# Optimization experiments

Measured on AMD Instinct MI355X. Metric: run time of the kernel, lower is better.

The kernel has to match this reference:

```python
import jax, jax.numpy as jnp
import numpy as np

SR = 4  # search_range
D = 2 * SR + 1  # 9
NC = D * D      # 81 output channels


def setup_inputs() -> dict:
    key = jax.random.key(0)
    k1, k2 = jax.random.split(key)
    B, C, H, W = 8, 64, 192, 256
    x1 = jax.random.normal(k1, (B, C, H, W), dtype=jnp.float32)
    x2 = jax.random.normal(k2, (B, C, H, W), dtype=jnp.float32)
    return {"x1": x1, "x2": x2}


def reference(x1, x2):
    B, C, H, W = x1.shape
    # Zero-pad x2 so out-of-overlap products are zero, matching the
    # zero-initialized cv in the original module.
    x2p = jnp.pad(x2, ((0, 0), (0, 0), (SR, SR), (SR, SR)))
    outs = [None] * NC
    for i in range(-SR, SR + 1):
        for j in range(-SR, SR + 1):
            # Original torch code uses cv[:, 9*i + j] with negative wraparound.
            k = (D * i + j) % NC
            # x2 sample position is (h - i, w - j); in padded coords start = SR - i.
            shifted = jax.lax.dynamic_slice(
                x2p, (0, 0, SR - i, SR - j), (B, C, H, W))
            outs[k] = jnp.sum(x1 * shifted, axis=1)  # [B, H, W]
    cv = jnp.stack(outs, axis=1)  # [B, 81, H, W]
    return cv / NC
```

## Files before the change

### kernel.cpp

```cpp
#include <hip/hip_runtime.h>

#define HH 192
#define WW 256
#define TH 8
#define TW 32
#define CCH 4
#define NCHUNK 16
#define THREADS 576
#define CHSTEP (CCH * HH * WW)

typedef float f4 __attribute__((ext_vector_type(4)));

#define GLL(gp, lp) __builtin_amdgcn_global_load_lds(                        \
    (const __attribute__((address_space(1))) unsigned int*)(gp),            \
    (__attribute__((address_space(3))) unsigned int*)(lp), 16, 0, 0)

__global__ __launch_bounds__(THREADS) void cost_volume_kernel(
    const float* __restrict__ x1, const float* __restrict__ x2,
    float* __restrict__ out)
{
    __shared__ __align__(16) float smem[10240];

    const int tid  = threadIdx.x;
    const int wave = tid >> 6;
    const int lane = tid & 63;
    const int r    = lane >> 3;
    const int wcg  = lane & 7;

    const int bid = blockIdx.x;
    const int b   = bid / 192;
    const int rem = bid % 192;
    const int h0  = (rem >> 3) * TH;
    const int w0  = (rem & 7) * TW;

    auto desc2 = [&](int u, bool& v, long& goff) {
        const int ch = u >> 8, row = (u >> 4) & 15, cu = u & 15;
        const int hg = h0 - 4 + row, wg = w0 - 4 + cu * 4;
        v = (cu <= 9) & (hg >= 0) & (hg < HH) & (wg >= 0) & (wg <= WW - 4);
        goff = ((long)(b * 64 + ch) * HH + hg) * WW + wg;
    };
    bool vA, vB0; long gA, gB;
    desc2((wave << 6) + lane, vA, gA);
    desc2(((wave + 9) << 6) + lane, vB0, gB);
    const bool vB = vB0 & (wave <= 6);

    const bool v1 = (wave >= 1) & (wave <= 4);
    const int w1 = (wave - 1) & 7;
    const int u1 = (w1 << 6) + lane;
    const int ch1 = u1 >> 6, r1 = (u1 >> 3) & 7, c1 = (u1 & 7) * 4;
    const long g1 = ((long)(b * 64 + ch1) * HH + (h0 + r1)) * WW + (w0 + c1);

    auto issue = [&](int nb, int n) {
        const long cofs = (long)n * CHSTEP;
        float* const b2 = smem + 2048 + nb * 4096;
        float* const b1 = smem + nb * 1024;
        if (vA) GLL(x2 + gA + cofs, b2 + (wave << 8));
        if (vB) GLL(x2 + gB + cofs, b2 + ((wave + 9) << 8));
        if (v1) GLL(x1 + g1 + cofs, b1 + (w1 << 8));
    };

    const f4 z4 = {0.f, 0.f, 0.f, 0.f};
    for (int z = tid; z < 10240 / 4; z += THREADS) ((f4*)smem)[z] = z4;
    __syncthreads();

    issue(0, 0);
    __syncthreads();

    f4 acc0 = z4, acc1 = z4, acc2 = z4, acc3 = z4, acc4 = z4,
       acc5 = z4, acc6 = z4, acc7 = z4, acc8 = z4;

    const int row2 = r + 8 - wave;

    for (int n = 0; n < NCHUNK; ++n) {
        if (n + 1 < NCHUNK) issue((n + 1) & 1, n + 1);
        const float* sb1 = smem + (n & 1) * 1024 + r * 32 + wcg * 4;
        const float* sb2 = smem + 2048 + (n & 1) * 4096 + row2 * 64 + wcg * 4;
#pragma unroll
        for (int cc = 0; cc < CCH; ++cc) {
            const f4 av  = *(const f4*)(sb1 + cc * 256);
            const f4 xv0 = *(const f4*)(sb2 + cc * 1024);
            const f4 xv1 = *(const f4*)(sb2 + cc * 1024 + 4);
            const f4 xv2 = *(const f4*)(sb2 + cc * 1024 + 8);
            const f4 w8 = xv0;
            const f4 w7 = __builtin_shufflevector(xv0, xv1, 1, 2, 3, 4);
            const f4 w6 = __builtin_shufflevector(xv0, xv1, 2, 3, 4, 5);
            const f4 w5 = __builtin_shufflevector(xv0, xv1, 3, 4, 5, 6);
            const f4 w4 = xv1;
            const f4 w3 = __builtin_shufflevector(xv1, xv2, 1, 2, 3, 4);
            const f4 w2 = __builtin_shufflevector(xv1, xv2, 2, 3, 4, 5);
            const f4 w1w = __builtin_shufflevector(xv1, xv2, 3, 4, 5, 6);
            const f4 w0w = xv2;
            acc0 = __builtin_elementwise_fma(av, w0w, acc0);
            acc1 = __builtin_elementwise_fma(av, w1w, acc1);
            acc2 = __builtin_elementwise_fma(av, w2, acc2);
            acc3 = __builtin_elementwise_fma(av, w3, acc3);
            acc4 = __builtin_elementwise_fma(av, w4, acc4);
            acc5 = __builtin_elementwise_fma(av, w5, acc5);
            acc6 = __builtin_elementwise_fma(av, w6, acc6);
            acc7 = __builtin_elementwise_fma(av, w7, acc7);
            acc8 = __builtin_elementwise_fma(av, w8, acc8);
        }
        __syncthreads();
    }

    const float scale = 1.0f / 81.0f;
    const int hout = h0 + r;
    const int wout = w0 + wcg * 4;
#define CV_OUT(JJ)                                                           \
    {                                                                        \
        const int k = (9 * wave + (JJ) + 41) % 81;                           \
        float* po = out + (((long)b * 81 + k) * HH + hout) * WW + wout;      \
        *(f4*)po = acc##JJ * scale;                                          \
    }
    CV_OUT(0) CV_OUT(1) CV_OUT(2) CV_OUT(3) CV_OUT(4)
    CV_OUT(5) CV_OUT(6) CV_OUT(7) CV_OUT(8)
#undef CV_OUT
}

extern "C" void kernel_launch(void* const* d_in, const int* in_sizes, int n_in,
                              void* d_out, int out_size, void* d_ws, size_t ws_size,
                              hipStream_t stream) {
    const float* x1 = (const float*)d_in[0];
    const float* x2 = (const float*)d_in[1];
    float* out = (float*)d_out;
    dim3 grid(8 * 24 * 8);
    dim3 block(THREADS);
    hipLaunchKernelGGL(cost_volume_kernel, grid, block, 0, stream, x1, x2, out);
}
```

Before: 115.8 us.

## Split cost-volume work per row-shift across blocks with full-width tiles

Each block now handles one vertical shift (i) across full 256-wide rows of an 8-row tile, so the 9 shifts go to 9 separate blocks instead of 9 waves in one block. x2 rows for that single shift are staged in LDS with a padded row layout, and x1 is read straight from global memory instead of LDS. The aim is to shrink the per-block x2 halo and LDS footprint, drop horizontal tile halos, and raise occupancy. The cost is that x1 is reloaded 9 times, once per shift block, which adds global and L2 traffic.

```diff
diff --git a/kernel.cpp b/kernel.cpp
--- a/kernel.cpp
+++ b/kernel.cpp
@@ -3,11 +3,14 @@
 #define HH 192
 #define WW 256
 #define TH 8
-#define TW 32
 #define CCH 4
 #define NCHUNK 16
-#define THREADS 576
+#define THREADS 512
 #define CHSTEP (CCH * HH * WW)
+#define ROWF 264
+#define CHF  (TH * ROWF)
+#define BUFF (CCH * CHF)
+#define UNITS_PER_CHUNK (CCH * TH * 66)
 
 typedef float f4 __attribute__((ext_vector_type(4)));
 
@@ -15,52 +18,52 @@
     (const __attribute__((address_space(1))) unsigned int*)(gp),            \
     (__attribute__((address_space(3))) unsigned int*)(lp), 16, 0, 0)
 
-__global__ __launch_bounds__(THREADS) void cost_volume_kernel(
+__global__ __attribute__((amdgpu_flat_work_group_size(512, 512),
+                          amdgpu_waves_per_eu(2, 4)))
+void cost_volume_kernel(
     const float* __restrict__ x1, const float* __restrict__ x2,
     float* __restrict__ out)
 {
-    __shared__ __align__(16) float smem[10240];
+    __shared__ __align__(16) float smem[2 * BUFF];
 
     const int tid  = threadIdx.x;
     const int wave = tid >> 6;
     const int lane = tid & 63;
-    const int r    = lane >> 3;
-    const int wcg  = lane & 7;
 
     const int bid = blockIdx.x;
-    const int b   = bid / 192;
-    const int rem = bid % 192;
-    const int h0  = (rem >> 3) * TH;
-    const int w0  = (rem & 7) * TW;
+    const int ib  = bid % 9;
+    const int ht  = (bid / 9) % 24;
+    const int b   = bid / 216;
+    const int h0  = ht * TH;
 
-    auto desc2 = [&](int u, bool& v, long& goff) {
-        const int ch = u >> 8, row = (u >> 4) & 15, cu = u & 15;
-        const int hg = h0 - 4 + row, wg = w0 - 4 + cu * 4;
-        v = (cu <= 9) & (hg >= 0) & (hg < HH) & (wg >= 0) & (wg <= WW - 4);
-        goff = ((long)(b * 64 + ch) * HH + hg) * WW + wg;
+    auto desc2 = [&](int s, int& goff) {
+        const int u = (s << 6) + lane;
+        const int ch = u / 528, rem = u % 528;
+        const int row = rem / 66, cu = rem % 66;
+        const int hg = h0 + row + 4 - ib;
+        const bool v = (cu >= 1) & (cu <= 64) & (hg >= 0) & (hg < HH);
+        goff = v ? (((b * 64 + ch) * HH + hg) * WW + (cu * 4 - 4)) : -1;
     };
-    bool vA, vB0; long gA, gB;
-    desc2((wave << 6) + lane, vA, gA);
-    desc2(((wave + 9) << 6) + lane, vB0, gB);
-    const bool vB = vB0 & (wave <= 6);
-
-    const bool v1 = (wave >= 1) & (wave <= 4);
-    const int w1 = (wave - 1) & 7;
-    const int u1 = (w1 << 6) + lane;
-    const int ch1 = u1 >> 6, r1 = (u1 >> 3) & 7, c1 = (u1 & 7) * 4;
-    const long g1 = ((long)(b * 64 + ch1) * HH + (h0 + r1)) * WW + (w0 + c1);
+    int gA, gB, gC, gD, gE;
+    desc2(wave,      gA);
+    desc2(wave + 8,  gB);
+    desc2(wave + 16, gC);
+    desc2(wave + 24, gD);
+    desc2(32,        gE);
+    const bool hE = (wave == 0);
 
     auto issue = [&](int nb, int n) {
-        const long cofs = (long)n * CHSTEP;
-        float* const b2 = smem + 2048 + nb * 4096;
-        float* const b1 = smem + nb * 1024;
-        if (vA) GLL(x2 + gA + cofs, b2 + (wave << 8));
-        if (vB) GLL(x2 + gB + cofs, b2 + ((wave + 9) << 8));
-        if (v1) GLL(x1 + g1 + cofs, b1 + (w1 << 8));
+        const int cofs = n * CHSTEP;
+        float* const base = smem + nb * BUFF;
+        if (gA >= 0) GLL(x2 + gA + cofs, base + (wave << 8));
+        if (gB >= 0) GLL(x2 + gB + cofs, base + ((wave + 8) << 8));
+        if (gC >= 0) GLL(x2 + gC + cofs, base + ((wave + 16) << 8));
+        if (gD >= 0) GLL(x2 + gD + cofs, base + ((wave + 24) << 8));
+        if (hE & (gE >= 0)) GLL(x2 + gE + cofs, base + (32 << 8));
     };
 
     const f4 z4 = {0.f, 0.f, 0.f, 0.f};
-    for (int z = tid; z < 10240 / 4; z += THREADS) ((f4*)smem)[z] = z4;
+    for (int z = tid; z < 2 * BUFF / 4; z += THREADS) ((f4*)smem)[z] = z4;
     __syncthreads();
 
     issue(0, 0);
@@ -69,18 +72,18 @@
     f4 acc0 = z4, acc1 = z4, acc2 = z4, acc3 = z4, acc4 = z4,
        acc5 = z4, acc6 = z4, acc7 = z4, acc8 = z4;
 
-    const int row2 = r + 8 - wave;
+    const float* x1p = x1 + ((long)(b * 64) * HH + (h0 + wave)) * WW + lane * 4;
 
     for (int n = 0; n < NCHUNK; ++n) {
         if (n + 1 < NCHUNK) issue((n + 1) & 1, n + 1);
-        const float* sb1 = smem + (n & 1) * 1024 + r * 32 + wcg * 4;
-        const float* sb2 = smem + 2048 + (n & 1) * 4096 + row2 * 64 + wcg * 4;
+        const float* sb2 = smem + (n & 1) * BUFF + wave * ROWF + lane * 4;
+        const float* x1c = x1p + (long)n * CHSTEP;
 #pragma unroll
         for (int cc = 0; cc < CCH; ++cc) {
-            const f4 av  = *(const f4*)(sb1 + cc * 256);
-            const f4 xv0 = *(const f4*)(sb2 + cc * 1024);
-            const f4 xv1 = *(const f4*)(sb2 + cc * 1024 + 4);
-            const f4 xv2 = *(const f4*)(sb2 + cc * 1024 + 8);
+            const f4 av  = *(const f4*)(x1c + cc * (HH * WW));
+            const f4 xv0 = *(const f4*)(sb2 + cc * CHF);
+            const f4 xv1 = *(const f4*)(sb2 + cc * CHF + 4);
+            const f4 xv2 = *(const f4*)(sb2 + cc * CHF + 8);
             const f4 w8 = xv0;
             const f4 w7 = __builtin_shufflevector(xv0, xv1, 1, 2, 3, 4);
             const f4 w6 = __builtin_shufflevector(xv0, xv1, 2, 3, 4, 5);
@@ -104,11 +107,11 @@
     }
 
     const float scale = 1.0f / 81.0f;
-    const int hout = h0 + r;
-    const int wout = w0 + wcg * 4;
+    const int hout = h0 + wave;
+    const int wout = lane * 4;
 #define CV_OUT(JJ)                                                           \
     {                                                                        \
-        const int k = (9 * wave + (JJ) + 41) % 81;                           \
+        const int k = (9 * ib + (JJ) + 41) % 81;                             \
         float* po = out + (((long)b * 81 + k) * HH + hout) * WW + wout;      \
         *(f4*)po = acc##JJ * scale;                                          \
     }
@@ -123,7 +126,7 @@
     const float* x1 = (const float*)d_in[0];
     const float* x2 = (const float*)d_in[1];
     float* out = (float*)d_out;
-    dim3 grid(8 * 24 * 8);
+    dim3 grid(8 * 24 * 9);
     dim3 block(THREADS);
     hipLaunchKernelGGL(cost_volume_kernel, grid, block, 0, stream, x1, x2, out);
 }
```

Result: slower. 231.6 us (+100.1%).
